# Kernel tuning notes

Measured on AMD Instinct MI355X. Metric: run time of the kernel, lower is better.

Reference implementation:

```python
import jax, jax.numpy as jnp
import numpy as np

N, D, R, E, B = 98304, 128, 3, 491520, 16384


def setup_inputs() -> dict:
    key = jax.random.key(0)
    ks = jax.random.split(key, 12)
    s = 0.05
    return {
        "latents": jax.random.normal(ks[0], (N, D), jnp.float32),
        "Wm": jax.random.normal(ks[1], (R, D, 2 * D), jnp.float32) * s,
        "bm": jax.random.normal(ks[2], (R, D), jnp.float32) * s,
        "W1": jax.random.normal(ks[3], (D, D), jnp.float32) * s,
        "b1": jax.random.normal(ks[4], (D,), jnp.float32) * s,
        "W2": jax.random.normal(ks[5], (D, D), jnp.float32) * s,
        "b2": jax.random.normal(ks[6], (D,), jnp.float32) * s,
        "message_from": jax.random.randint(ks[7], (E,), 0, N),
        "message_to": jax.random.randint(ks[8], (E,), 0, N),
        "view_id": jax.random.randint(ks[9], (N,), 0, B),
        "ch": 6,
        "batch_size": B,
    }


def reference(latents, Wm, bm, W1, b1, W2, b2, message_from, message_to, view_id, ch, batch_size):
    # Message passing rounds: gather -> concat -> Linear+ReLU (dropout=identity in eval) -> scale -> scatter-add
    scale = 1.0 / (ch - 1)
    for r in range(Wm.shape[0]):
        h = jnp.concatenate([latents[message_from], latents[message_to]], axis=-1)  # [E, 2D]
        msg = jax.nn.relu(h @ Wm[r].T + bm[r]) * scale  # [E, D]
        latents = latents.at[message_to].add(msg)
    # Readout: sum latents per sample (note: original's `/ ch` result is discarded, so no division)
    y = jax.ops.segment_sum(latents, view_id, num_segments=batch_size)  # [B, D]
    h = jax.nn.relu(y @ W1.T + b1)
    return h @ W2.T + b2
```

## Files before the change

kernel.cpp:

```cpp
#include <hip/hip_runtime.h>

static constexpr int N  = 98304;
static constexpr int D  = 128;
static constexpr int E  = 491520;
static constexpr int B  = 16384;

using f32x4 = __attribute__((ext_vector_type(4))) float;
using s16x8 = __attribute__((ext_vector_type(8))) short;

__device__ __forceinline__ ushort f2bf(float x) {
    unsigned u = __float_as_uint(x);
    return (ushort)((u + 0x7fffu + ((u >> 16) & 1u)) >> 16);
}
__device__ __forceinline__ float bflo(unsigned u) { return __uint_as_float(u << 16); }
__device__ __forceinline__ float bfhi(unsigned u) { return __uint_as_float(u & 0xffff0000u); }

__global__ void zero_kernel(float* __restrict__ p, int n) {
    int i = blockIdx.x * blockDim.x + threadIdx.x;
    int stride = gridDim.x * blockDim.x;
    for (; i < n; i += stride) p[i] = 0.f;
}

__global__ void zero_int_kernel(int* __restrict__ p, int n) {
    int i = blockIdx.x * blockDim.x + threadIdx.x;
    int stride = gridDim.x * blockDim.x;
    for (; i < n; i += stride) p[i] = 0;
}


__global__ void hist_kernel(const int* __restrict__ eto, int* __restrict__ cnt) {
    int e = blockIdx.x * 256 + threadIdx.x;
    if (e < E) atomicAdd(&cnt[eto[e]], 1);
}

__global__ __launch_bounds__(256) void scan1_kernel(const int* __restrict__ cnt,
                                                    int* __restrict__ excl, int* __restrict__ bsum) {
    __shared__ int s[256];
    const int b = blockIdx.x, t = threadIdx.x;
    const int base = b * 1024 + t * 4;
    int4 v = *reinterpret_cast<const int4*>(cnt + base);
    int local = v.x + v.y + v.z + v.w;
    s[t] = local; __syncthreads();
    for (int off = 1; off < 256; off <<= 1) {
        int x = (t >= off) ? s[t - off] : 0;
        __syncthreads();
        s[t] += x;
        __syncthreads();
    }
    int excl_t = s[t] - local;
    if (t == 255) bsum[b] = s[t];
    int4 o;
    o.x = excl_t; o.y = o.x + v.x; o.z = o.y + v.y; o.w = o.z + v.z;
    *reinterpret_cast<int4*>(excl + base) = o;
}

__global__ void scan2_kernel(int* __restrict__ bsum, int nb) {
    if (threadIdx.x == 0) {
        int run = 0;
        for (int i = 0; i < nb; ++i) { int v = bsum[i]; bsum[i] = run; run += v; }
    }
}

__global__ void scan3_kernel(int* __restrict__ excl, const int* __restrict__ bsum) {
    int i = blockIdx.x * 256 + threadIdx.x;
    excl[i] += bsum[i >> 10];
}

__global__ void scatter_kernel(const int* __restrict__ efrom, const int* __restrict__ eto,
                               int* __restrict__ cursor, int* __restrict__ sfrom) {
    int e = blockIdx.x * 256 + threadIdx.x;
    if (e >= E) return;
    int p = atomicAdd(&cursor[eto[e]], 1);
    sfrom[p] = efrom[e];
}

__global__ void convUV_kernel(const float* __restrict__ Wm, ushort* __restrict__ Wf) {
    int gid = blockIdx.x * 256 + threadIdx.x;
    if (gid >= 3 * 32768) return;
    int r = gid >> 15, rem = gid & 32767;
    int j = rem & 7, lane = (rem >> 3) & 63, grp = rem >> 9;
    int kt = grp >> 4, nt = grp & 15;
    int n = (nt & 7) * 16 + (lane & 15);
    int k = kt * 32 + (lane >> 4) * 8 + j;
    int col = ((nt >> 3) << 7) + k;
    Wf[gid] = f2bf(Wm[((size_t)r * 128 + n) * 256 + col]);
}

__global__ void convW12_kernel(const float* __restrict__ W1, const float* __restrict__ W2,
                               ushort* __restrict__ Wb12) {
    int gid = blockIdx.x * 256 + threadIdx.x;
    if (gid >= 2 * 16384) return;
    int w = gid >> 14, rem = gid & 16383;
    int n = rem >> 7, k = rem & 127;
    int kt = k >> 5, nt = n >> 4;
    int lane = (n & 15) + (((k >> 3) & 3) << 4);
    int j = k & 7;
    const float* W = w ? W2 : W1;
    Wb12[w * 16384 + ((kt * 8 + nt) * 64 + lane) * 8 + j] = f2bf(W[rem]);
}

__global__ __launch_bounds__(256) void uv_kernel(
    const float* __restrict__ Asrc,
    ushort* __restrict__ Z,
    const ushort* __restrict__ Wft,
    const float* __restrict__ bm_r)
{
    const int t = threadIdx.x;
    const int wave = t >> 6, lane = t & 63;
    const int col16 = lane & 15, kq = lane >> 4;
    const int arow = blockIdx.x * 64 + wave * 16 + col16;

    const float4* Ar = reinterpret_cast<const float4*>(Asrc + (size_t)arow * 128);
    f32x4 acc[16];
    #pragma unroll
    for (int nt = 0; nt < 16; ++nt) acc[nt] = (f32x4){0.f, 0.f, 0.f, 0.f};

    const s16x8* wf = reinterpret_cast<const s16x8*>(Wft);
    #pragma unroll
    for (int kt = 0; kt < 4; ++kt) {
        float4 a0 = Ar[kt * 8 + kq * 2];
        float4 a1 = Ar[kt * 8 + kq * 2 + 1];
        union { s16x8 v; ushort u[8]; } pk;
        pk.u[0] = f2bf(a0.x); pk.u[1] = f2bf(a0.y); pk.u[2] = f2bf(a0.z); pk.u[3] = f2bf(a0.w);
        pk.u[4] = f2bf(a1.x); pk.u[5] = f2bf(a1.y); pk.u[6] = f2bf(a1.z); pk.u[7] = f2bf(a1.w);
        #pragma unroll
        for (int nt = 0; nt < 16; ++nt)
            acc[nt] = __builtin_amdgcn_mfma_f32_16x16x32_bf16(pk.v, wf[(kt * 16 + nt) * 64 + lane], acc[nt], 0, 0, 0);
    }

    const int rbase = blockIdx.x * 64 + wave * 16 + kq * 4;
    #pragma unroll
    for (int nt = 0; nt < 16; ++nt) {
        float bias = (nt >= 8) ? bm_r[(nt - 8) * 16 + col16] : 0.f;
        int cfull = ((nt >> 3) << 7) + (nt & 7) * 16 + col16;
        #pragma unroll
        for (int j = 0; j < 4; ++j)
            Z[(size_t)(rbase + j) * 256 + cfull] = f2bf(acc[nt][j] + bias);
    }
}

__global__ __launch_bounds__(256) void edge_sum_kernel(
    const ushort* __restrict__ Z,
    const float* __restrict__ Lsrc,
    float* __restrict__ Ldst,
    const int* __restrict__ sfrom,
    const int* __restrict__ ends,
    const int* __restrict__ ch_ptr)
{
    const int t = threadIdx.x;
    const int wave = t >> 6, lane = t & 63;
    const int v = blockIdx.x * 4 + wave;
    const int lo = (v == 0) ? 0 : ends[v - 1];
    const int hi = ends[v];
    const float scale = 1.0f / (float)(ch_ptr[0] - 1);

    unsigned vv = *reinterpret_cast<const unsigned*>(Z + (size_t)v * 256 + 128 + lane * 2);
    const float v0 = bflo(vv), v1 = bfhi(vv);

    float a0 = 0.f, a1 = 0.f;
    int e = lo;
    for (; e + 2 <= hi; e += 2) {
        int f0 = sfrom[e], f1 = sfrom[e + 1];
        unsigned u0 = *reinterpret_cast<const unsigned*>(Z + (size_t)f0 * 256 + lane * 2);
        unsigned u1 = *reinterpret_cast<const unsigned*>(Z + (size_t)f1 * 256 + lane * 2);
        a0 += fmaxf(bflo(u0) + v0, 0.f) + fmaxf(bflo(u1) + v0, 0.f);
        a1 += fmaxf(bfhi(u0) + v1, 0.f) + fmaxf(bfhi(u1) + v1, 0.f);
    }
    if (e < hi) {
        int f0 = sfrom[e];
        unsigned u0 = *reinterpret_cast<const unsigned*>(Z + (size_t)f0 * 256 + lane * 2);
        a0 += fmaxf(bflo(u0) + v0, 0.f);
        a1 += fmaxf(bfhi(u0) + v1, 0.f);
    }

    float2 lold = *reinterpret_cast<const float2*>(Lsrc + (size_t)v * 128 + lane * 2);
    float2 out;
    out.x = lold.x + scale * a0;
    out.y = lold.y + scale * a1;
    *reinterpret_cast<float2*>(Ldst + (size_t)v * 128 + lane * 2) = out;
}

__global__ __launch_bounds__(128) void segsum_kernel(
    const float* __restrict__ lat, const int* __restrict__ view, float* __restrict__ y)
{
    const int n = blockIdx.x;
    const int v = view[n];
    atomicAdd(&y[(size_t)v * D + threadIdx.x], lat[(size_t)n * D + threadIdx.x]);
}

__global__ __launch_bounds__(256) void readout_mfma_kernel(
    float* __restrict__ y,
    const ushort* __restrict__ Wb1, const ushort* __restrict__ Wb2,
    const float* __restrict__ b1, const float* __restrict__ b2)
{
    __shared__ alignas(16) ushort hs[64 * 128];
    const int t = threadIdx.x;
    const int r0 = blockIdx.x * 64;
    char* hbase = reinterpret_cast<char*>(hs);
    const float4* y4 = reinterpret_cast<const float4*>(y);

    #pragma unroll
    for (int it = 0; it < 4; ++it) {
        int c = t + it * 256;
        int e = c >> 4, p = c & 15;
        int g = p ^ (e & 15);
        float4 a = y4[(size_t)(r0 + e) * 32 + g * 2];
        float4 bq = y4[(size_t)(r0 + e) * 32 + g * 2 + 1];
        union { s16x8 v; ushort u[8]; } pk;
        pk.u[0] = f2bf(a.x); pk.u[1] = f2bf(a.y); pk.u[2] = f2bf(a.z); pk.u[3] = f2bf(a.w);
        pk.u[4] = f2bf(bq.x); pk.u[5] = f2bf(bq.y); pk.u[6] = f2bf(bq.z); pk.u[7] = f2bf(bq.w);
        *reinterpret_cast<s16x8*>(hbase + e * 256 + p * 16) = pk.v;
    }
    __syncthreads();

    const int wave = t >> 6, lane = t & 63;
    const int rrow = wave * 16 + (lane & 15);
    const int kq = lane >> 4;
    const int rx = rrow & 15;
    const char* hrow = hbase + rrow * 256;
    const int col16 = lane & 15;

    f32x4 acc[8];
    #pragma unroll
    for (int nt = 0; nt < 8; ++nt) acc[nt] = (f32x4){0.f, 0.f, 0.f, 0.f};
    const s16x8* wf1 = reinterpret_cast<const s16x8*>(Wb1);
    #pragma unroll
    for (int kt = 0; kt < 4; ++kt) {
        int C = kt * 4 + kq;
        s16x8 a = *reinterpret_cast<const s16x8*>(hrow + ((C ^ rx) & 15) * 16);
        #pragma unroll
        for (int nt = 0; nt < 8; ++nt)
            acc[nt] = __builtin_amdgcn_mfma_f32_16x16x32_bf16(a, wf1[(kt * 8 + nt) * 64 + lane], acc[nt], 0, 0, 0);
    }
    __syncthreads();

    #pragma unroll
    for (int nt = 0; nt < 8; ++nt) {
        float bias = b1[nt * 16 + col16];
        #pragma unroll
        for (int j = 0; j < 4; ++j) {
            int r = wave * 16 + (lane >> 4) * 4 + j;
            float h = fmaxf(acc[nt][j] + bias, 0.f);
            int colfull = nt * 16 + col16;
            int chunk = colfull >> 3;
            int bo = ((chunk ^ (r & 15)) * 16) + (colfull & 7) * 2;
            *reinterpret_cast<ushort*>(hbase + r * 256 + bo) = f2bf(h);
        }
    }
    __syncthreads();

    f32x4 acc2[8];
    #pragma unroll
    for (int nt = 0; nt < 8; ++nt) acc2[nt] = (f32x4){0.f, 0.f, 0.f, 0.f};
    const s16x8* wf2 = reinterpret_cast<const s16x8*>(Wb2);
    #pragma unroll
    for (int kt = 0; kt < 4; ++kt) {
        int C = kt * 4 + kq;
        s16x8 a = *reinterpret_cast<const s16x8*>(hrow + ((C ^ rx) & 15) * 16);
        #pragma unroll
        for (int nt = 0; nt < 8; ++nt)
            acc2[nt] = __builtin_amdgcn_mfma_f32_16x16x32_bf16(a, wf2[(kt * 8 + nt) * 64 + lane], acc2[nt], 0, 0, 0);
    }

    #pragma unroll
    for (int nt = 0; nt < 8; ++nt) {
        float bias = b2[nt * 16 + col16];
        #pragma unroll
        for (int j = 0; j < 4; ++j) {
            int r = r0 + wave * 16 + (lane >> 4) * 4 + j;
            y[(size_t)r * 128 + nt * 16 + col16] = acc2[nt][j] + bias;
        }
    }
}

extern "C" void kernel_launch(void* const* d_in, const int* in_sizes, int n_in,
                              void* d_out, int out_size, void* d_ws, size_t ws_size,
                              hipStream_t stream) {
    const float* latents = (const float*)d_in[0];
    const float* Wm      = (const float*)d_in[1];
    const float* bm      = (const float*)d_in[2];
    const float* W1      = (const float*)d_in[3];
    const float* b1      = (const float*)d_in[4];
    const float* W2      = (const float*)d_in[5];
    const float* b2      = (const float*)d_in[6];
    const int*   efrom   = (const int*)d_in[7];
    const int*   eto     = (const int*)d_in[8];
    const int*   view    = (const int*)d_in[9];
    const int*   ch      = (const int*)d_in[10];

    float*  L = (float*)d_ws;
    ushort* Z = (ushort*)(L + (size_t)N * D);

    char* ob = (char*)d_out;
    ushort* WUVf = (ushort*)ob;
    int*    cnt   = (int*)(ob + 196608);
    int*    excl  = cnt + N;
    int*    bsum  = excl + N;
    int*    sfrom = bsum + 128;
    float*  out   = (float*)d_out;

    convUV_kernel<<<384, 256, 0, stream>>>(Wm, WUVf);
    zero_int_kernel<<<384, 256, 0, stream>>>(cnt, N);
    hist_kernel<<<E / 256, 256, 0, stream>>>(eto, cnt);
    scan1_kernel<<<N / 1024, 256, 0, stream>>>(cnt, excl, bsum);
    scan2_kernel<<<1, 64, 0, stream>>>(bsum, N / 1024);
    scan3_kernel<<<N / 256, 256, 0, stream>>>(excl, bsum);
    scatter_kernel<<<E / 256, 256, 0, stream>>>(efrom, eto, excl, sfrom);

    uv_kernel<<<N / 64, 256, 0, stream>>>(latents, Z, WUVf, bm);
    edge_sum_kernel<<<N / 4, 256, 0, stream>>>(Z, latents, L, sfrom, excl, ch);
    uv_kernel<<<N / 64, 256, 0, stream>>>(L, Z, WUVf + 32768, bm + D);
    edge_sum_kernel<<<N / 4, 256, 0, stream>>>(Z, L, L, sfrom, excl, ch);
    uv_kernel<<<N / 64, 256, 0, stream>>>(L, Z, WUVf + 65536, bm + 2 * D);
    edge_sum_kernel<<<N / 4, 256, 0, stream>>>(Z, L, L, sfrom, excl, ch);

    ushort* Wb12 = Z;
    convW12_kernel<<<128, 256, 0, stream>>>(W1, W2, Wb12);
    zero_kernel<<<2048, 256, 0, stream>>>(out, B * D);
    segsum_kernel<<<N, 128, 0, stream>>>(L, view, out);
    readout_mfma_kernel<<<256, 256, 0, stream>>>(out, Wb12, Wb12 + 16384, b1, b2);
}
```

Baseline: 351.9 us.

## Replace atomic segment-sum with sorted CSR gather and batch graph preprocessing

The readout segment sum now sorts nodes by view_id through a counting sort that shares the edge CSR's histogram, scan and scatter kernels, and reduces each segment with a gather instead of float atomics. This drops the zero-fill and the N-block atomic kernel. The edge-sum kernel now handles four nodes per wave with a 4-way unrolled, masked gather loop, and uv_kernel loads all of its A-row data up front. The cost is extra workspace (perm, vcnt, vexcl), a larger preprocessing pass, and a summation order that differs from the atomic version.

```diff
diff --git a/kernel.cpp b/kernel.cpp
--- a/kernel.cpp
+++ b/kernel.cpp
@@ -15,30 +15,27 @@
 __device__ __forceinline__ float bflo(unsigned u) { return __uint_as_float(u << 16); }
 __device__ __forceinline__ float bfhi(unsigned u) { return __uint_as_float(u & 0xffff0000u); }
 
-__global__ void zero_kernel(float* __restrict__ p, int n) {
-    int i = blockIdx.x * blockDim.x + threadIdx.x;
-    int stride = gridDim.x * blockDim.x;
-    for (; i < n; i += stride) p[i] = 0.f;
-}
-
-__global__ void zero_int_kernel(int* __restrict__ p, int n) {
-    int i = blockIdx.x * blockDim.x + threadIdx.x;
-    int stride = gridDim.x * blockDim.x;
-    for (; i < n; i += stride) p[i] = 0;
-}
-
-
-__global__ void hist_kernel(const int* __restrict__ eto, int* __restrict__ cnt) {
-    int e = blockIdx.x * 256 + threadIdx.x;
-    if (e < E) atomicAdd(&cnt[eto[e]], 1);
-}
-
-__global__ __launch_bounds__(256) void scan1_kernel(const int* __restrict__ cnt,
-                                                    int* __restrict__ excl, int* __restrict__ bsum) {
+__global__ void zero2_kernel(int* __restrict__ p) {
+    int i = blockIdx.x * 256 + threadIdx.x;
+    if (i < N + B) p[i] = 0;
+}
+
+__global__ void hist2_kernel(const int* __restrict__ eto, const int* __restrict__ view,
+                             int* __restrict__ cnt, int* __restrict__ vcnt) {
+    int gid = blockIdx.x * 256 + threadIdx.x;
+    if (gid < E) atomicAdd(&cnt[eto[gid]], 1);
+    else if (gid < E + N) atomicAdd(&vcnt[view[gid - E]], 1);
+}
+
+__global__ __launch_bounds__(256) void scan1_kernel(const int* __restrict__ cnt, int* __restrict__ excl,
+                                                    const int* __restrict__ vcnt, int* __restrict__ vexcl,
+                                                    int* __restrict__ bsum) {
     __shared__ int s[256];
     const int b = blockIdx.x, t = threadIdx.x;
-    const int base = b * 1024 + t * 4;
-    int4 v = *reinterpret_cast<const int4*>(cnt + base);
+    const int* src; int* dst; int base;
+    if (b < 96) { src = cnt;  dst = excl;  base = b * 1024 + t * 4; }
+    else        { src = vcnt; dst = vexcl; base = (b - 96) * 1024 + t * 4; }
+    int4 v = *reinterpret_cast<const int4*>(src + base);
     int local = v.x + v.y + v.z + v.w;
     s[t] = local; __syncthreads();
     for (int off = 1; off < 256; off <<= 1) {
@@ -51,27 +48,35 @@
     if (t == 255) bsum[b] = s[t];
     int4 o;
     o.x = excl_t; o.y = o.x + v.x; o.z = o.y + v.y; o.w = o.z + v.z;
-    *reinterpret_cast<int4*>(excl + base) = o;
-}
-
-__global__ void scan2_kernel(int* __restrict__ bsum, int nb) {
-    if (threadIdx.x == 0) {
-        int run = 0;
-        for (int i = 0; i < nb; ++i) { int v = bsum[i]; bsum[i] = run; run += v; }
-    }
-}
-
-__global__ void scan3_kernel(int* __restrict__ excl, const int* __restrict__ bsum) {
-    int i = blockIdx.x * 256 + threadIdx.x;
-    excl[i] += bsum[i >> 10];
-}
-
-__global__ void scatter_kernel(const int* __restrict__ efrom, const int* __restrict__ eto,
-                               int* __restrict__ cursor, int* __restrict__ sfrom) {
-    int e = blockIdx.x * 256 + threadIdx.x;
-    if (e >= E) return;
-    int p = atomicAdd(&cursor[eto[e]], 1);
-    sfrom[p] = efrom[e];
+    *reinterpret_cast<int4*>(dst + base) = o;
+}
+
+__global__ void scan2_kernel(int* __restrict__ bsum) {
+    int t = threadIdx.x;
+    if (t == 0) { int run = 0; for (int i = 0;  i < 96;  ++i) { int v = bsum[i]; bsum[i] = run; run += v; } }
+    if (t == 1) { int run = 0; for (int i = 96; i < 112; ++i) { int v = bsum[i]; bsum[i] = run; run += v; } }
+}
+
+__global__ void scan3_kernel(int* __restrict__ excl, int* __restrict__ vexcl,
+                             const int* __restrict__ bsum) {
+    int b = blockIdx.x, t = threadIdx.x;
+    if (b < 384) { int i = b * 256 + t; excl[i] += bsum[i >> 10]; }
+    else         { int i = (b - 384) * 256 + t; vexcl[i] += bsum[96 + (i >> 10)]; }
+}
+
+__global__ void scatter2_kernel(const int* __restrict__ efrom, const int* __restrict__ eto,
+                                const int* __restrict__ view,
+                                int* __restrict__ ecur, int* __restrict__ vcur,
+                                int* __restrict__ sfrom, int* __restrict__ perm) {
+    int gid = blockIdx.x * 256 + threadIdx.x;
+    if (gid < E) {
+        int p = atomicAdd(&ecur[eto[gid]], 1);
+        sfrom[p] = efrom[gid];
+    } else if (gid < E + N) {
+        int n = gid - E;
+        int p = atomicAdd(&vcur[view[n]], 1);
+        perm[p] = n;
+    }
 }
 
 __global__ void convUV_kernel(const float* __restrict__ Wm, ushort* __restrict__ Wf) {
@@ -100,10 +105,8 @@
 }
 
 __global__ __launch_bounds__(256) void uv_kernel(
-    const float* __restrict__ Asrc,
-    ushort* __restrict__ Z,
-    const ushort* __restrict__ Wft,
-    const float* __restrict__ bm_r)
+    const float* __restrict__ Asrc, ushort* __restrict__ Z,
+    const ushort* __restrict__ Wft, const float* __restrict__ bm_r)
 {
     const int t = threadIdx.x;
     const int wave = t >> 6, lane = t & 63;
@@ -111,6 +114,13 @@
     const int arow = blockIdx.x * 64 + wave * 16 + col16;
 
     const float4* Ar = reinterpret_cast<const float4*>(Asrc + (size_t)arow * 128);
+    float4 areg[8];
+    #pragma unroll
+    for (int kt = 0; kt < 4; ++kt) {
+        areg[2 * kt]     = Ar[kt * 8 + kq * 2];
+        areg[2 * kt + 1] = Ar[kt * 8 + kq * 2 + 1];
+    }
+
     f32x4 acc[16];
     #pragma unroll
     for (int nt = 0; nt < 16; ++nt) acc[nt] = (f32x4){0.f, 0.f, 0.f, 0.f};
@@ -118,8 +128,7 @@
     const s16x8* wf = reinterpret_cast<const s16x8*>(Wft);
     #pragma unroll
     for (int kt = 0; kt < 4; ++kt) {
-        float4 a0 = Ar[kt * 8 + kq * 2];
-        float4 a1 = Ar[kt * 8 + kq * 2 + 1];
+        float4 a0 = areg[2 * kt], a1 = areg[2 * kt + 1];
         union { s16x8 v; ushort u[8]; } pk;
         pk.u[0] = f2bf(a0.x); pk.u[1] = f2bf(a0.y); pk.u[2] = f2bf(a0.z); pk.u[3] = f2bf(a0.w);
         pk.u[4] = f2bf(a1.x); pk.u[5] = f2bf(a1.y); pk.u[6] = f2bf(a1.z); pk.u[7] = f2bf(a1.w);
@@ -140,56 +149,77 @@
 }
 
 __global__ __launch_bounds__(256) void edge_sum_kernel(
-    const ushort* __restrict__ Z,
-    const float* __restrict__ Lsrc,
-    float* __restrict__ Ldst,
-    const int* __restrict__ sfrom,
-    const int* __restrict__ ends,
-    const int* __restrict__ ch_ptr)
+    const ushort* __restrict__ Z, const float* __restrict__ Lsrc, float* __restrict__ Ldst,
+    const int* __restrict__ sfrom, const int* __restrict__ ends, const int* __restrict__ ch_ptr)
+{
+    const int t = threadIdx.x;
+    const int wave = t >> 6, lane = t & 63;
+    const float scale = 1.0f / (float)(ch_ptr[0] - 1);
+
+    #pragma unroll
+    for (int i = 0; i < 4; ++i) {
+        const int v = blockIdx.x * 16 + wave * 4 + i;
+        const int lo = (v == 0) ? 0 : ends[v - 1];
+        const int hi = ends[v];
+
+        unsigned vv = *reinterpret_cast<const unsigned*>(Z + (size_t)v * 256 + 128 + lane * 2);
+        const float v0 = bflo(vv), v1 = bfhi(vv);
+
+        float a0 = 0.f, a1 = 0.f;
+        for (int e = lo; e < hi; e += 4) {
+            int last = hi - 1;
+            int e1 = (e + 1 < hi) ? e + 1 : last;
+            int e2 = (e + 2 < hi) ? e + 2 : last;
+            int e3 = (e + 3 < hi) ? e + 3 : last;
+            float m1 = (e + 1 < hi) ? 1.f : 0.f;
+            float m2 = (e + 2 < hi) ? 1.f : 0.f;
+            float m3 = (e + 3 < hi) ? 1.f : 0.f;
+            int f0 = sfrom[e], f1 = sfrom[e1], f2 = sfrom[e2], f3 = sfrom[e3];
+            unsigned u0 = *reinterpret_cast<const unsigned*>(Z + (size_t)f0 * 256 + lane * 2);
+            unsigned u1 = *reinterpret_cast<const unsigned*>(Z + (size_t)f1 * 256 + lane * 2);
+            unsigned u2 = *reinterpret_cast<const unsigned*>(Z + (size_t)f2 * 256 + lane * 2);
+            unsigned u3 = *reinterpret_cast<const unsigned*>(Z + (size_t)f3 * 256 + lane * 2);
+            a0 += fmaxf(bflo(u0) + v0, 0.f) + m1 * fmaxf(bflo(u1) + v0, 0.f)
+                + m2 * fmaxf(bflo(u2) + v0, 0.f) + m3 * fmaxf(bflo(u3) + v0, 0.f);
+            a1 += fmaxf(bfhi(u0) + v1, 0.f) + m1 * fmaxf(bfhi(u1) + v1, 0.f)
+                + m2 * fmaxf(bfhi(u2) + v1, 0.f) + m3 * fmaxf(bfhi(u3) + v1, 0.f);
+        }
+
+        float2 lold = *reinterpret_cast<const float2*>(Lsrc + (size_t)v * 128 + lane * 2);
+        float2 outv;
+        outv.x = lold.x + scale * a0;
+        outv.y = lold.y + scale * a1;
+        *reinterpret_cast<float2*>(Ldst + (size_t)v * 128 + lane * 2) = outv;
+    }
+}
+
+__global__ __launch_bounds__(256) void segsum_sorted_kernel(
+    const float* __restrict__ L, const int* __restrict__ perm,
+    const int* __restrict__ vends, float* __restrict__ y)
 {
     const int t = threadIdx.x;
     const int wave = t >> 6, lane = t & 63;
     const int v = blockIdx.x * 4 + wave;
-    const int lo = (v == 0) ? 0 : ends[v - 1];
-    const int hi = ends[v];
-    const float scale = 1.0f / (float)(ch_ptr[0] - 1);
-
-    unsigned vv = *reinterpret_cast<const unsigned*>(Z + (size_t)v * 256 + 128 + lane * 2);
-    const float v0 = bflo(vv), v1 = bfhi(vv);
+    const int lo = (v == 0) ? 0 : vends[v - 1];
+    const int hi = vends[v];
 
     float a0 = 0.f, a1 = 0.f;
-    int e = lo;
-    for (; e + 2 <= hi; e += 2) {
-        int f0 = sfrom[e], f1 = sfrom[e + 1];
-        unsigned u0 = *reinterpret_cast<const unsigned*>(Z + (size_t)f0 * 256 + lane * 2);
-        unsigned u1 = *reinterpret_cast<const unsigned*>(Z + (size_t)f1 * 256 + lane * 2);
-        a0 += fmaxf(bflo(u0) + v0, 0.f) + fmaxf(bflo(u1) + v0, 0.f);
-        a1 += fmaxf(bfhi(u0) + v1, 0.f) + fmaxf(bfhi(u1) + v1, 0.f);
-    }
-    if (e < hi) {
-        int f0 = sfrom[e];
-        unsigned u0 = *reinterpret_cast<const unsigned*>(Z + (size_t)f0 * 256 + lane * 2);
-        a0 += fmaxf(bflo(u0) + v0, 0.f);
-        a1 += fmaxf(bfhi(u0) + v1, 0.f);
-    }
-
-    float2 lold = *reinterpret_cast<const float2*>(Lsrc + (size_t)v * 128 + lane * 2);
-    float2 out;
-    out.x = lold.x + scale * a0;
-    out.y = lold.y + scale * a1;
-    *reinterpret_cast<float2*>(Ldst + (size_t)v * 128 + lane * 2) = out;
-}
-
-__global__ __launch_bounds__(128) void segsum_kernel(
-    const float* __restrict__ lat, const int* __restrict__ view, float* __restrict__ y)
-{
-    const int n = blockIdx.x;
-    const int v = view[n];
-    atomicAdd(&y[(size_t)v * D + threadIdx.x], lat[(size_t)n * D + threadIdx.x]);
+    for (int e = lo; e < hi; e += 2) {
+        int last = hi - 1;
+        int e1 = (e + 1 < hi) ? e + 1 : last;
+        float m1 = (e + 1 < hi) ? 1.f : 0.f;
+        int n0 = perm[e], n1 = perm[e1];
+        float2 x0 = *reinterpret_cast<const float2*>(L + (size_t)n0 * 128 + lane * 2);
+        float2 x1 = *reinterpret_cast<const float2*>(L + (size_t)n1 * 128 + lane * 2);
+        a0 += x0.x + m1 * x1.x;
+        a1 += x0.y + m1 * x1.y;
+    }
+    float2 o; o.x = a0; o.y = a1;
+    *reinterpret_cast<float2*>(y + (size_t)v * 128 + lane * 2) = o;
 }
 
 __global__ __launch_bounds__(256) void readout_mfma_kernel(
-    float* __restrict__ y,
+    const float* __restrict__ y, float* __restrict__ outp,
     const ushort* __restrict__ Wb1, const ushort* __restrict__ Wb2,
     const float* __restrict__ b1, const float* __restrict__ b2)
 {
@@ -268,7 +298,7 @@
         #pragma unroll
         for (int j = 0; j < 4; ++j) {
             int r = r0 + wave * 16 + (lane >> 4) * 4 + j;
-            y[(size_t)r * 128 + nt * 16 + col16] = acc2[nt][j] + bias;
+            outp[(size_t)r * 128 + nt * 16 + col16] = acc2[nt][j] + bias;
         }
     }
 }
@@ -288,35 +318,38 @@
     const int*   view    = (const int*)d_in[9];
     const int*   ch      = (const int*)d_in[10];
 
-    float*  L = (float*)d_ws;
-    ushort* Z = (ushort*)(L + (size_t)N * D);
+    float*  L  = (float*)d_ws;
+    ushort* Z  = (ushort*)(L + (size_t)N * D);
+    float*  yb = (float*)Z;
+    ushort* Wb12 = (ushort*)((char*)Z + 8388608);
 
     char* ob = (char*)d_out;
     ushort* WUVf = (ushort*)ob;
-    int*    cnt   = (int*)(ob + 196608);
-    int*    excl  = cnt + N;
-    int*    bsum  = excl + N;
-    int*    sfrom = bsum + 128;
-    float*  out   = (float*)d_out;
+    int* cnt   = (int*)(ob + 196608);
+    int* vcnt  = cnt + N;
+    int* excl  = vcnt + B;
+    int* vexcl = excl + N;
+    int* bsum  = vexcl + B;
+    int* sfrom = bsum + 128;
+    int* perm  = sfrom + E;
+    float* outp = (float*)d_out;
 
     convUV_kernel<<<384, 256, 0, stream>>>(Wm, WUVf);
-    zero_int_kernel<<<384, 256, 0, stream>>>(cnt, N);
-    hist_kernel<<<E / 256, 256, 0, stream>>>(eto, cnt);
-    scan1_kernel<<<N / 1024, 256, 0, stream>>>(cnt, excl, bsum);
-    scan2_kernel<<<1, 64, 0, stream>>>(bsum, N / 1024);
-    scan3_kernel<<<N / 256, 256, 0, stream>>>(excl, bsum);
-    scatter_kernel<<<E / 256, 256, 0, stream>>>(efrom, eto, excl, sfrom);
+    zero2_kernel<<<(N + B) / 256, 256, 0, stream>>>(cnt);
+    hist2_kernel<<<(E + N) / 256, 256, 0, stream>>>(eto, view, cnt, vcnt);
+    scan1_kernel<<<112, 256, 0, stream>>>(cnt, excl, vcnt, vexcl, bsum);
+    scan2_kernel<<<1, 64, 0, stream>>>(bsum);
+    scan3_kernel<<<448, 256, 0, stream>>>(excl, vexcl, bsum);
+    scatter2_kernel<<<(E + N) / 256, 256, 0, stream>>>(efrom, eto, view, excl, vexcl, sfrom, perm);
 
     uv_kernel<<<N / 64, 256, 0, stream>>>(latents, Z, WUVf, bm);
-    edge_sum_kernel<<<N / 4, 256, 0, stream>>>(Z, latents, L, sfrom, excl, ch);
+    edge_sum_kernel<<<N / 16, 256, 0, stream>>>(Z, latents, L, sfrom, excl, ch);
     uv_kernel<<<N / 64, 256, 0, stream>>>(L, Z, WUVf + 32768, bm + D);
-    edge_sum_kernel<<<N / 4, 256, 0, stream>>>(Z, L, L, sfrom, excl, ch);
+    edge_sum_kernel<<<N / 16, 256, 0, stream>>>(Z, L, L, sfrom, excl, ch);
     uv_kernel<<<N / 64, 256, 0, stream>>>(L, Z, WUVf + 65536, bm + 2 * D);
-    edge_sum_kernel<<<N / 4, 256, 0, stream>>>(Z, L, L, sfrom, excl, ch);
-
-    ushort* Wb12 = Z;
+    edge_sum_kernel<<<N / 16, 256, 0, stream>>>(Z, L, L, sfrom, excl, ch);
+
     convW12_kernel<<<128, 256, 0, stream>>>(W1, W2, Wb12);
-    zero_kernel<<<2048, 256, 0, stream>>>(out, B * D);
-    segsum_kernel<<<N, 128, 0, stream>>>(L, view, out);
-    readout_mfma_kernel<<<256, 256, 0, stream>>>(out, Wb12, Wb12 + 16384, b1, b2);
-}
+    segsum_sorted_kernel<<<B / 4, 256, 0, stream>>>(L, perm, vexcl, yb);
+    readout_mfma_kernel<<<B / 64, 256, 0, stream>>>(yb, outp, Wb12, Wb12 + 16384, b1, b2);
+}
```

Result: faster. 307.8 us (-12.5%).
